# Kernel tuning notes

Measured on AMD Instinct MI355X. Metric: run time of the kernel, lower is better.

Reference implementation:

```python
import jax, jax.numpy as jnp
import numpy as np

VOCAB, IN, MEM, HID, CLS = 50000, 512, 512, 512, 5
N, K = 512, 4  # nodes per tree, max children (complete 4-ary tree)


def _build_children(n, k):
    # Complete k-ary heap, relabeled j = n-1-i so every child index < its parent
    # index (topological order for the scan). Pad missing children with n, which
    # indexes a permanent zero row in the state buffers (matches torch's zero
    # child_c/child_h for leaves: f*0 contributes nothing).
    ch = np.full((n, k), n, dtype=np.int32)
    for j in range(n):
        i = n - 1 - j
        for m in range(1, k + 1):
            c = k * i + m
            if c <= n - 1:
                ch[j, m - 1] = n - 1 - c
    return jnp.asarray(ch)


def setup_inputs() -> dict:
    key = jax.random.key(0)
    ks = jax.random.split(key, 16)
    s_in, s_mem, s_2m, s_h = IN ** -0.5, MEM ** -0.5, (2 * MEM) ** -0.5, HID ** -0.5
    emb = jax.random.normal(ks[0], (VOCAB, IN), jnp.float32)
    emb = emb.at[0].set(0.0)  # padding_idx=0
    inp = {
        "linputs": jax.random.randint(ks[1], (N,), 1, VOCAB, jnp.int32),
        "rinputs": jax.random.randint(ks[2], (N,), 1, VOCAB, jnp.int32),
        "lchildren": _build_children(N, K),
        "rchildren": _build_children(N, K),
        "emb": emb,
        "W_ioux": jax.random.normal(ks[3], (IN, 3 * MEM), jnp.float32) * s_in,
        "b_ioux": jnp.zeros((3 * MEM,), jnp.float32),
        "W_iouh": jax.random.normal(ks[4], (MEM, 3 * MEM), jnp.float32) * s_mem,
        "b_iouh": jnp.zeros((3 * MEM,), jnp.float32),
        "W_fx": jax.random.normal(ks[5], (IN, MEM), jnp.float32) * s_in,
        "b_fx": jnp.zeros((MEM,), jnp.float32),
        "W_fh": jax.random.normal(ks[6], (MEM, MEM), jnp.float32) * s_mem,
        "b_fh": jnp.zeros((MEM,), jnp.float32),
        "Wh": jax.random.normal(ks[7], (2 * MEM, HID), jnp.float32) * s_2m,
        "bh": jnp.zeros((HID,), jnp.float32),
        "Wp": jax.random.normal(ks[8], (HID, CLS), jnp.float32) * s_h,
        "bp": jnp.zeros((CLS,), jnp.float32),
    }
    return inp


def _childsum_encode(tokens, children, emb, W_ioux, b_ioux, W_iouh, b_iouh,
                     W_fx, b_fx, W_fh, b_fh):
    n, mem = tokens.shape[0], W_fh.shape[0]
    x = emb[tokens]                       # [N, IN]
    xiou = x @ W_ioux + b_ioux            # [N, 3M]  (input part, hoisted)
    xf = x @ W_fx + b_fx                  # [N, M]
    c0 = jnp.zeros((n + 1, mem), x.dtype)  # row n = permanent zero state
    h0 = jnp.zeros((n + 1, mem), x.dtype)

    def step(carry, inp):
        c_all, h_all = carry
        i, xiou_i, xf_i, ch = inp
        cc = c_all[ch]                    # [K, M]
        hh = h_all[ch]                    # [K, M]
        iou = xiou_i + hh.sum(0) @ W_iouh + b_iouh
        ig, og, ug = jnp.split(iou, 3)
        ig, og, ug = jax.nn.sigmoid(ig), jax.nn.sigmoid(og), jnp.tanh(ug)
        f = jax.nn.sigmoid(hh @ W_fh + b_fh + xf_i)   # [K, M]
        c = ig * ug + (f * cc).sum(0)
        h = og * jnp.tanh(c)
        return (c_all.at[i].set(c), h_all.at[i].set(h)), None

    idx = jnp.arange(n)
    (c_all, h_all), _ = jax.lax.scan(step, (c0, h0), (idx, xiou, xf, children))
    return c_all[n - 1][None, :], h_all[n - 1][None, :]  # root (c, h)


def reference(linputs, rinputs, lchildren, rchildren, emb,
              W_ioux, b_ioux, W_iouh, b_iouh, W_fx, b_fx, W_fh, b_fh,
              Wh, bh, Wp, bp):
    lc, _ = _childsum_encode(linputs, lchildren, emb, W_ioux, b_ioux,
                             W_iouh, b_iouh, W_fx, b_fx, W_fh, b_fh)
    rc, _ = _childsum_encode(rinputs, rchildren, emb, W_ioux, b_ioux,
                             W_iouh, b_iouh, W_fx, b_fx, W_fh, b_fh)
    # Similarity head (note: the torch model feeds CELL states lstate/rstate)
    vec = jnp.concatenate([lc * rc, jnp.abs(lc - rc)], axis=1)  # [1, 2M]
    hid = jax.nn.sigmoid(vec @ Wh + bh)
    return jax.nn.log_softmax(hid @ Wp + bp, axis=1)            # [1, CLS]
```

## Files before the change

### kernel.cpp

```cpp
#include <hip/hip_runtime.h>
#include <hip/hip_bf16.h>
#include <math.h>


typedef __attribute__((ext_vector_type(8))) __bf16 bf16x8;
typedef __attribute__((ext_vector_type(4))) float f32x4;

__device__ __forceinline__ float sigm(float x) { return 1.0f / (1.0f + __expf(-x)); }

__device__ __forceinline__ unsigned short f2bf(float f) {
    union { float f; unsigned int u; } v; v.f = f;
    unsigned int r = v.u + 0x7FFF + ((v.u >> 16) & 1);
    return (unsigned short)(r >> 16);
}
__device__ __forceinline__ float bf2f(unsigned short b) {
    union { unsigned int u; float f; } v; v.u = ((unsigned int)b) << 16;
    return v.f;
}
__device__ __forceinline__ f32x4 mfma16(bf16x8 a, bf16x8 b, f32x4 c) {
    return __builtin_amdgcn_mfma_f32_16x16x32_bf16(a, b, c, 0, 0, 0);
}
__device__ __forceinline__ bf16x8 load_f32_as_bf8(const float* p) {
    float4 x = *(const float4*)p;
    float4 y = *(const float4*)(p + 4);
    bf16x8 r;
    r[0] = (__bf16)x.x; r[1] = (__bf16)x.y; r[2] = (__bf16)x.z; r[3] = (__bf16)x.w;
    r[4] = (__bf16)y.x; r[5] = (__bf16)y.y; r[6] = (__bf16)y.z; r[7] = (__bf16)y.w;
    return r;
}

__device__ __forceinline__
void ttile(const float* __restrict__ src, int lds_, unsigned short* __restrict__ dst,
           int ldd, int k0, int n0, float (*ts)[33], int tid)
{
    const int tx = tid & 31, ty = tid >> 5;
#pragma unroll
    for (int i = 0; i < 4; ++i)
        ts[ty + 8 * i][tx] = src[(size_t)(k0 + ty + 8 * i) * lds_ + n0 + tx];
    __syncthreads();
#pragma unroll
    for (int i = 0; i < 4; ++i)
        dst[(size_t)(n0 + ty + 8 * i) * ldd + k0 + tx] = f2bf(ts[tx][ty + 8 * i]);
}

__global__ __launch_bounds__(256)
void prep(const float* __restrict__ W_iouh, const float* __restrict__ W_fh,
          const float* __restrict__ W_ioux, const float* __restrict__ W_fx,
          const float* __restrict__ Wh,
          unsigned short* __restrict__ WiouhT, unsigned short* __restrict__ WfhT,
          unsigned short* __restrict__ WxT, unsigned short* __restrict__ Whb,
          unsigned short* __restrict__ hbf, float* __restrict__ cbuf,
          float* __restrict__ hid_raw)
{
    __shared__ float ts[32][33];
    const int t = blockIdx.x, tid = threadIdx.x;
    if (t < 768) {
        ttile(W_iouh, 1536, WiouhT, 512, (t & 15) * 32, (t >> 4) * 32, ts, tid);
    } else if (t < 1024) {
        const int tt = t - 768;
        ttile(W_fh, 512, WfhT, 512, (tt & 15) * 32, (tt >> 4) * 32, ts, tid);
    } else if (t < 1792) {
        const int tt = t - 1024;
        ttile(W_ioux, 1536, WxT, 512, (tt & 15) * 32, (tt >> 4) * 32, ts, tid);
    } else if (t < 2048) {
        const int tt = t - 1792;
        ttile(W_fx, 512, WxT + (size_t)1536 * 512, 512, (tt & 15) * 32, (tt >> 4) * 32, ts, tid);
    } else if (t < 2304) {
        size_t base = (size_t)(t - 2048) * 2048 + tid;
#pragma unroll
        for (int i = 0; i < 8; ++i) Whb[base + 256 * i] = f2bf(Wh[base + 256 * i]);
    } else {
        for (int i = tid; i < 512; i += 256) {
            hbf[(size_t)512 * 512 + i] = 0;
            hbf[(size_t)1025 * 512 + i] = 0;
            cbuf[(size_t)512 * 512 + i] = 0.f;
            cbuf[(size_t)1025 * 512 + i] = 0.f;
            hid_raw[i] = 0.f;
        }
    }
}

__global__ __launch_bounds__(256)
void prege(const float* __restrict__ emb, const int* __restrict__ lin,
           const int* __restrict__ rin, const unsigned short* __restrict__ WxT,
           const float* __restrict__ b_ioux, const float* __restrict__ b_fx,
           unsigned short* __restrict__ xcat)
{
    const int mt = blockIdx.x & 31, nb = blockIdx.x >> 5;
    const int tid = threadIdx.x, w = tid >> 6, lane = tid & 63;
    const int m = lane & 15, q = lane >> 4;
    const int colbase = nb * 256 + w * 64;
    const int r0 = mt * 32 + m, r1 = r0 + 16;
    const int tok0 = (r0 < 512) ? lin[r0] : rin[r0 - 512];
    const int tok1 = (r1 < 512) ? lin[r1] : rin[r1 - 512];
    const float* A0 = emb + (size_t)tok0 * 512;
    const float* A1 = emb + (size_t)tok1 * 512;

    f32x4 acc[2][4];
#pragma unroll
    for (int i = 0; i < 2; ++i)
#pragma unroll
        for (int j = 0; j < 4; ++j) acc[i][j] = (f32x4){0.f, 0.f, 0.f, 0.f};

    for (int k0 = 0; k0 < 512; k0 += 32) {
        const int koff = k0 + q * 8;
        bf16x8 a0 = load_f32_as_bf8(A0 + koff);
        bf16x8 a1 = load_f32_as_bf8(A1 + koff);
#pragma unroll
        for (int jj = 0; jj < 4; ++jj) {
            bf16x8 b = *(const bf16x8*)(WxT + (size_t)(colbase + jj * 16 + m) * 512 + koff);
            acc[0][jj] = mfma16(a0, b, acc[0][jj]);
            acc[1][jj] = mfma16(a1, b, acc[1][jj]);
        }
    }
#pragma unroll
    for (int i = 0; i < 2; ++i)
#pragma unroll
        for (int jj = 0; jj < 4; ++jj)
#pragma unroll
            for (int rr = 0; rr < 4; ++rr) {
                const int R = mt * 32 + i * 16 + q * 4 + rr;
                const int col = colbase + jj * 16 + m;
                const float bias = (col < 1536) ? b_ioux[col] : b_fx[col - 1536];
                xcat[(size_t)R * 2048 + col] = f2bf(acc[i][jj][rr] + bias);
            }
}

__global__ __launch_bounds__(256)
void phase_gemm(const unsigned short* __restrict__ hbf,
                const int* __restrict__ lch, const int* __restrict__ rch,
                const unsigned short* __restrict__ WiouhT,
                const unsigned short* __restrict__ WfhT,
                const float* __restrict__ b_iouh, const float* __restrict__ b_fh,
                const unsigned short* __restrict__ xcat,
                float* __restrict__ ioub, float* __restrict__ fpre,
                int lo, int B, int nti1, int mti1, int mti2)
{
    const int B2 = 2 * B;
    const int tid = threadIdx.x, w = tid >> 6, lane = tid & 63;
    const int m = lane & 15, q = lane >> 4;
    int t = blockIdx.x;

    if (t < nti1) {
        const int mt = t % mti1, nb = t / mti1;
        const int colbase = nb * 256 + w * 64;
        const unsigned short* pA[2][4];
#pragma unroll
        for (int i = 0; i < 2; ++i) {
            const int r = mt * 32 + m + i * 16;
            int c[4] = {512, 512, 512, 512};
            int tree = 0;
            if (r < B2) {
                tree = (r >= B) ? 1 : 0;
                const int j = lo + r - tree * B;
                const int* ch = (tree ? rch : lch) + 4 * j;
                c[0] = ch[0]; c[1] = ch[1]; c[2] = ch[2]; c[3] = ch[3];
            }
            const unsigned short* hb = hbf + (size_t)tree * 513 * 512;
#pragma unroll
            for (int s = 0; s < 4; ++s) pA[i][s] = hb + (size_t)c[s] * 512;
        }
        f32x4 acc[2][4];
#pragma unroll
        for (int i = 0; i < 2; ++i)
#pragma unroll
            for (int j = 0; j < 4; ++j) acc[i][j] = (f32x4){0.f, 0.f, 0.f, 0.f};

        for (int k0 = 0; k0 < 512; k0 += 32) {
            const int koff = k0 + q * 8;
            bf16x8 af[2];
#pragma unroll
            for (int i = 0; i < 2; ++i) {
                float s[8] = {0.f, 0.f, 0.f, 0.f, 0.f, 0.f, 0.f, 0.f};
#pragma unroll
                for (int cc = 0; cc < 4; ++cc) {
                    bf16x8 v = *(const bf16x8*)(pA[i][cc] + koff);
#pragma unroll
                    for (int j = 0; j < 8; ++j) s[j] += (float)v[j];
                }
                bf16x8 a;
#pragma unroll
                for (int j = 0; j < 8; ++j) a[j] = (__bf16)s[j];
                af[i] = a;
            }
#pragma unroll
            for (int jj = 0; jj < 4; ++jj) {
                bf16x8 b = *(const bf16x8*)(WiouhT + (size_t)(colbase + jj * 16 + m) * 512 + koff);
                acc[0][jj] = mfma16(af[0], b, acc[0][jj]);
                acc[1][jj] = mfma16(af[1], b, acc[1][jj]);
            }
        }
#pragma unroll
        for (int i = 0; i < 2; ++i)
#pragma unroll
            for (int jj = 0; jj < 4; ++jj)
#pragma unroll
                for (int rr = 0; rr < 4; ++rr) {
                    const int R = mt * 32 + i * 16 + q * 4 + rr;
                    if (R < B2) {
                        const int tr = (R >= B) ? 1 : 0;
                        const int jR = lo + R - tr * B;
                        const int col = colbase + jj * 16 + m;
                        ioub[(size_t)R * 1536 + col] = acc[i][jj][rr] + b_iouh[col]
                            + bf2f(xcat[(size_t)(tr * 512 + jR) * 2048 + col]);
                    }
                }
    } else {
        t -= nti1;
        const int mt = t % mti2, nb = t / mti2;
        const int colbase = nb * 256 + w * 64;
        const unsigned short* pA[2];
#pragma unroll
        for (int i = 0; i < 2; ++i) {
            const int rf = mt * 32 + m + i * 16;
            int tree = 0, c = 512;
            if (rf < 4 * B2) {
                const int r = rf >> 2, s = rf & 3;
                tree = (r >= B) ? 1 : 0;
                const int j = lo + r - tree * B;
                c = ((tree ? rch : lch) + 4 * j)[s];
            }
            pA[i] = hbf + ((size_t)tree * 513 + c) * 512;
        }
        f32x4 acc[2][4];
#pragma unroll
        for (int i = 0; i < 2; ++i)
#pragma unroll
            for (int j = 0; j < 4; ++j) acc[i][j] = (f32x4){0.f, 0.f, 0.f, 0.f};

        for (int k0 = 0; k0 < 512; k0 += 32) {
            const int koff = k0 + q * 8;
            bf16x8 a0 = *(const bf16x8*)(pA[0] + koff);
            bf16x8 a1 = *(const bf16x8*)(pA[1] + koff);
#pragma unroll
            for (int jj = 0; jj < 4; ++jj) {
                bf16x8 b = *(const bf16x8*)(WfhT + (size_t)(colbase + jj * 16 + m) * 512 + koff);
                acc[0][jj] = mfma16(a0, b, acc[0][jj]);
                acc[1][jj] = mfma16(a1, b, acc[1][jj]);
            }
        }
#pragma unroll
        for (int i = 0; i < 2; ++i)
#pragma unroll
            for (int jj = 0; jj < 4; ++jj)
#pragma unroll
                for (int rr = 0; rr < 4; ++rr) {
                    const int R = mt * 32 + i * 16 + q * 4 + rr;
                    if (R < 4 * B2) {
                        const int rR = R >> 2;
                        const int tr = (rR >= B) ? 1 : 0;
                        const int jR = lo + rR - tr * B;
                        const int col = colbase + jj * 16 + m;
                        fpre[(size_t)R * 512 + col] = acc[i][jj][rr] + b_fh[col]
                            + bf2f(xcat[(size_t)(tr * 512 + jR) * 2048 + 1536 + col]);
                    }
                }
    }
}

__global__ __launch_bounds__(256)
void gating_k(const float* __restrict__ ioub, const float* __restrict__ fpre,
              const int* __restrict__ lch, const int* __restrict__ rch,
              float* __restrict__ cbuf, unsigned short* __restrict__ hbf,
              int lo, int B)
{
    const int r = blockIdx.x;
    const int tree = (r >= B) ? 1 : 0;
    const int j = lo + r - tree * B;
    const int* ch = (tree ? rch : lch) + 4 * j;
    const int c0 = ch[0], c1 = ch[1], c2 = ch[2], c3 = ch[3];
    float* cb = cbuf + (size_t)tree * 513 * 512;
    unsigned short* hb = hbf + (size_t)tree * 513 * 512;
    const float* ir = ioub + (size_t)r * 1536;
    const float* fr = fpre + (size_t)r * 4 * 512;
#pragma unroll
    for (int u = 0; u < 2; ++u) {
        const int col = threadIdx.x + u * 256;
        const float ig = sigm(ir[col]);
        const float og = sigm(ir[512 + col]);
        const float ug = tanhf(ir[1024 + col]);
        float cv = ig * ug
            + sigm(fr[col])        * cb[(size_t)c0 * 512 + col]
            + sigm(fr[512 + col])  * cb[(size_t)c1 * 512 + col]
            + sigm(fr[1024 + col]) * cb[(size_t)c2 * 512 + col]
            + sigm(fr[1536 + col]) * cb[(size_t)c3 * 512 + col];
        cb[(size_t)j * 512 + col] = cv;
        hb[(size_t)j * 512 + col] = f2bf(og * tanhf(cv));
    }
}

__global__ __launch_bounds__(256)
void head1(const float* __restrict__ cbuf, const unsigned short* __restrict__ Whb,
           float* __restrict__ hid_raw)
{
    __shared__ float red[4][64];
    const float* lc = cbuf + (size_t)511 * 512;
    const float* rc = cbuf + (size_t)(513 + 511) * 512;
    const int tid = threadIdx.x, w = tid >> 6, lane = tid & 63;
    const int cg = blockIdx.x & 7, kg = blockIdx.x >> 3;
    const int col = cg * 64 + lane;
    const int kbase = kg * 128 + w * 32;
    float acc = 0.f;
#pragma unroll 8
    for (int i = 0; i < 32; ++i) {
        const int k = kbase + i;
        float v;
        if (k < 512) v = lc[k] * rc[k];
        else { const int kk = k - 512; v = fabsf(lc[kk] - rc[kk]); }
        acc += v * bf2f(Whb[(size_t)k * 512 + col]);
    }
    red[w][lane] = acc;
    __syncthreads();
    if (w == 0)
        atomicAdd(&hid_raw[col], red[0][lane] + red[1][lane] + red[2][lane] + red[3][lane]);
}

__global__ __launch_bounds__(256)
void head2(const float* __restrict__ hid_raw, const float* __restrict__ bh,
           const float* __restrict__ Wp, const float* __restrict__ bp,
           float* __restrict__ out)
{
    __shared__ float red[4][5];
    const int tid = threadIdx.x, w = tid >> 6, lane = tid & 63;
    float a[5] = {0.f, 0.f, 0.f, 0.f, 0.f};
    for (int k = tid; k < 512; k += 256) {
        const float hv = sigm(hid_raw[k] + bh[k]);
#pragma unroll
        for (int cc = 0; cc < 5; ++cc) a[cc] += hv * Wp[(size_t)k * 5 + cc];
    }
#pragma unroll
    for (int cc = 0; cc < 5; ++cc)
        for (int off = 32; off; off >>= 1) a[cc] += __shfl_xor(a[cc], off, 64);
    if (lane == 0)
#pragma unroll
        for (int cc = 0; cc < 5; ++cc) red[w][cc] = a[cc];
    __syncthreads();
    if (tid == 0) {
        float lg[5], mx = -1e30f;
#pragma unroll
        for (int cc = 0; cc < 5; ++cc) {
            lg[cc] = red[0][cc] + red[1][cc] + red[2][cc] + red[3][cc] + bp[cc];
            mx = fmaxf(mx, lg[cc]);
        }
        float s = 0.f;
#pragma unroll
        for (int cc = 0; cc < 5; ++cc) s += __expf(lg[cc] - mx);
        const float lse = mx + __logf(s);
#pragma unroll
        for (int cc = 0; cc < 5; ++cc) out[cc] = lg[cc] - lse;
    }
}

extern "C" void kernel_launch(void* const* d_in, const int* in_sizes, int n_in,
                              void* d_out, int out_size, void* d_ws, size_t ws_size,
                              hipStream_t stream)
{
    const int*   lin     = (const int*)d_in[0];
    const int*   rin     = (const int*)d_in[1];
    const int*   lch     = (const int*)d_in[2];
    const int*   rch     = (const int*)d_in[3];
    const float* emb     = (const float*)d_in[4];
    const float* W_ioux  = (const float*)d_in[5];
    const float* b_ioux  = (const float*)d_in[6];
    const float* W_iouh  = (const float*)d_in[7];
    const float* b_iouh  = (const float*)d_in[8];
    const float* W_fx    = (const float*)d_in[9];
    const float* b_fx    = (const float*)d_in[10];
    const float* W_fh    = (const float*)d_in[11];
    const float* b_fh    = (const float*)d_in[12];
    const float* Wh      = (const float*)d_in[13];
    const float* bh      = (const float*)d_in[14];
    const float* Wp      = (const float*)d_in[15];
    const float* bp      = (const float*)d_in[16];
    float* out = (float*)d_out;
    (void)ws_size; (void)n_in; (void)in_sizes; (void)out_size;

    char* p = (char*)d_ws;
    unsigned short* WiouhT = (unsigned short*)p;            p += (size_t)1536 * 512 * 2;
    unsigned short* WfhT   = (unsigned short*)p;            p += (size_t)512 * 512 * 2;
    unsigned short* WxT    = (unsigned short*)p;            p += (size_t)2048 * 512 * 2;
    unsigned short* Whb    = (unsigned short*)p;            p += (size_t)1024 * 512 * 2;
    unsigned short* xcat   = (unsigned short*)p;            p += (size_t)1024 * 2048 * 2;
    unsigned short* hbf    = (unsigned short*)p;            p += (size_t)2 * 513 * 512 * 2;
    float*          cbuf   = (float*)p;                     p += (size_t)2 * 513 * 512 * 4;
    float*          ioub   = (float*)p;                     p += (size_t)512 * 1536 * 4;
    float*          fpre   = (float*)p;                     p += (size_t)2048 * 512 * 4;
    float*          hid_raw= (float*)p;                     p += (size_t)512 * 4;

    prep<<<2305, 256, 0, stream>>>(W_iouh, W_fh, W_ioux, W_fx, Wh,
                                   WiouhT, WfhT, WxT, Whb, hbf, cbuf, hid_raw);
    prege<<<256, 256, 0, stream>>>(emb, lin, rin, WxT, b_ioux, b_fx, xcat);

    static const int los[6] = {0, 171, 427, 491, 507, 511};
    static const int his[6] = {171, 427, 491, 507, 511, 512};
    for (int ph = 0; ph < 6; ++ph) {
        const int lo = los[ph], B = his[ph] - los[ph], B2 = 2 * B;
        const int mti1 = (B2 + 31) / 32;
        const int mti2 = (4 * B2 + 31) / 32;
        const int nti1 = mti1 * 6;
        const int nti2 = mti2 * 2;
        phase_gemm<<<nti1 + nti2, 256, 0, stream>>>(hbf, lch, rch, WiouhT, WfhT,
                                                    b_iouh, b_fh, xcat, ioub, fpre,
                                                    lo, B, nti1, mti1, mti2);
        gating_k<<<B2, 256, 0, stream>>>(ioub, fpre, lch, rch, cbuf, hbf, lo, B);
    }

    head1<<<64, 256, 0, stream>>>(cbuf, Whb, hid_raw);
    head2<<<1, 256, 0, stream>>>(hid_raw, bh, Wp, bp, out);
}
```

Measured before the change: 397.0 us.

## Fuse all phases into one cooperative persistent kernel with grid syncs

Replaces the sequence of about 16 kernel launches (prep, embedding GEMM, six phase GEMM/gating pairs, two head kernels) with a single cooperative kernel of 256 blocks that separates stages with grid.sync. It also special-cases the leaf phase, whose children are all zero, so it is computed directly from xcat without any GEMM. The final root gating and the classifier head run in one block. This removes launch gaps, but grid-wide barriers have their own cost, and the grid-strided loops can use the machine less fully than the old per-stage grid sizes did.

```diff
diff --git a/kernel.cpp b/kernel.cpp
--- a/kernel.cpp
+++ b/kernel.cpp
@@ -1,10 +1,14 @@
 #include <hip/hip_runtime.h>
-#include <hip/hip_bf16.h>
+#include <hip/hip_cooperative_groups.h>
 #include <math.h>
+
+namespace cg = cooperative_groups;
 
 
 typedef __attribute__((ext_vector_type(8))) __bf16 bf16x8;
 typedef __attribute__((ext_vector_type(4))) float f32x4;
+
+#define GRID 256
 
 __device__ __forceinline__ float sigm(float x) { return 1.0f / (1.0f + __expf(-x)); }
 
@@ -29,6 +33,16 @@
     return r;
 }
 
+struct Args {
+    const int   *lin, *rin, *lch, *rch;
+    const float *emb;
+    const float *W_ioux, *b_ioux, *W_iouh, *b_iouh;
+    const float *W_fx, *b_fx, *W_fh, *b_fh;
+    const float *Wh, *bh, *Wp, *bp;
+    unsigned short *WiouhT, *WfhT, *WxT, *Whb, *xcat, *hbf;
+    float *cbuf, *ioub, *fpre, *out;
+};
+
 __device__ __forceinline__
 void ttile(const float* __restrict__ src, int lds_, unsigned short* __restrict__ dst,
            int ldd, int k0, int n0, float (*ts)[33], int tid)
@@ -43,103 +57,12 @@
         dst[(size_t)(n0 + ty + 8 * i) * ldd + k0 + tx] = f2bf(ts[tx][ty + 8 * i]);
 }
 
-__global__ __launch_bounds__(256)
-void prep(const float* __restrict__ W_iouh, const float* __restrict__ W_fh,
-          const float* __restrict__ W_ioux, const float* __restrict__ W_fx,
-          const float* __restrict__ Wh,
-          unsigned short* __restrict__ WiouhT, unsigned short* __restrict__ WfhT,
-          unsigned short* __restrict__ WxT, unsigned short* __restrict__ Whb,
-          unsigned short* __restrict__ hbf, float* __restrict__ cbuf,
-          float* __restrict__ hid_raw)
-{
-    __shared__ float ts[32][33];
-    const int t = blockIdx.x, tid = threadIdx.x;
-    if (t < 768) {
-        ttile(W_iouh, 1536, WiouhT, 512, (t & 15) * 32, (t >> 4) * 32, ts, tid);
-    } else if (t < 1024) {
-        const int tt = t - 768;
-        ttile(W_fh, 512, WfhT, 512, (tt & 15) * 32, (tt >> 4) * 32, ts, tid);
-    } else if (t < 1792) {
-        const int tt = t - 1024;
-        ttile(W_ioux, 1536, WxT, 512, (tt & 15) * 32, (tt >> 4) * 32, ts, tid);
-    } else if (t < 2048) {
-        const int tt = t - 1792;
-        ttile(W_fx, 512, WxT + (size_t)1536 * 512, 512, (tt & 15) * 32, (tt >> 4) * 32, ts, tid);
-    } else if (t < 2304) {
-        size_t base = (size_t)(t - 2048) * 2048 + tid;
-#pragma unroll
-        for (int i = 0; i < 8; ++i) Whb[base + 256 * i] = f2bf(Wh[base + 256 * i]);
-    } else {
-        for (int i = tid; i < 512; i += 256) {
-            hbf[(size_t)512 * 512 + i] = 0;
-            hbf[(size_t)1025 * 512 + i] = 0;
-            cbuf[(size_t)512 * 512 + i] = 0.f;
-            cbuf[(size_t)1025 * 512 + i] = 0.f;
-            hid_raw[i] = 0.f;
-        }
-    }
-}
-
-__global__ __launch_bounds__(256)
-void prege(const float* __restrict__ emb, const int* __restrict__ lin,
-           const int* __restrict__ rin, const unsigned short* __restrict__ WxT,
-           const float* __restrict__ b_ioux, const float* __restrict__ b_fx,
-           unsigned short* __restrict__ xcat)
-{
-    const int mt = blockIdx.x & 31, nb = blockIdx.x >> 5;
-    const int tid = threadIdx.x, w = tid >> 6, lane = tid & 63;
-    const int m = lane & 15, q = lane >> 4;
-    const int colbase = nb * 256 + w * 64;
-    const int r0 = mt * 32 + m, r1 = r0 + 16;
-    const int tok0 = (r0 < 512) ? lin[r0] : rin[r0 - 512];
-    const int tok1 = (r1 < 512) ? lin[r1] : rin[r1 - 512];
-    const float* A0 = emb + (size_t)tok0 * 512;
-    const float* A1 = emb + (size_t)tok1 * 512;
-
-    f32x4 acc[2][4];
-#pragma unroll
-    for (int i = 0; i < 2; ++i)
-#pragma unroll
-        for (int j = 0; j < 4; ++j) acc[i][j] = (f32x4){0.f, 0.f, 0.f, 0.f};
-
-    for (int k0 = 0; k0 < 512; k0 += 32) {
-        const int koff = k0 + q * 8;
-        bf16x8 a0 = load_f32_as_bf8(A0 + koff);
-        bf16x8 a1 = load_f32_as_bf8(A1 + koff);
-#pragma unroll
-        for (int jj = 0; jj < 4; ++jj) {
-            bf16x8 b = *(const bf16x8*)(WxT + (size_t)(colbase + jj * 16 + m) * 512 + koff);
-            acc[0][jj] = mfma16(a0, b, acc[0][jj]);
-            acc[1][jj] = mfma16(a1, b, acc[1][jj]);
-        }
-    }
-#pragma unroll
-    for (int i = 0; i < 2; ++i)
-#pragma unroll
-        for (int jj = 0; jj < 4; ++jj)
-#pragma unroll
-            for (int rr = 0; rr < 4; ++rr) {
-                const int R = mt * 32 + i * 16 + q * 4 + rr;
-                const int col = colbase + jj * 16 + m;
-                const float bias = (col < 1536) ? b_ioux[col] : b_fx[col - 1536];
-                xcat[(size_t)R * 2048 + col] = f2bf(acc[i][jj][rr] + bias);
-            }
-}
-
-__global__ __launch_bounds__(256)
-void phase_gemm(const unsigned short* __restrict__ hbf,
-                const int* __restrict__ lch, const int* __restrict__ rch,
-                const unsigned short* __restrict__ WiouhT,
-                const unsigned short* __restrict__ WfhT,
-                const float* __restrict__ b_iouh, const float* __restrict__ b_fh,
-                const unsigned short* __restrict__ xcat,
-                float* __restrict__ ioub, float* __restrict__ fpre,
-                int lo, int B, int nti1, int mti1, int mti2)
+__device__ __forceinline__
+void gemm_task(int t, int lo, int B, int mti1, int nti1, int mti2, const Args& a)
 {
     const int B2 = 2 * B;
     const int tid = threadIdx.x, w = tid >> 6, lane = tid & 63;
     const int m = lane & 15, q = lane >> 4;
-    int t = blockIdx.x;
 
     if (t < nti1) {
         const int mt = t % mti1, nb = t / mti1;
@@ -153,10 +76,10 @@
             if (r < B2) {
                 tree = (r >= B) ? 1 : 0;
                 const int j = lo + r - tree * B;
-                const int* ch = (tree ? rch : lch) + 4 * j;
+                const int* ch = (tree ? a.rch : a.lch) + 4 * j;
                 c[0] = ch[0]; c[1] = ch[1]; c[2] = ch[2]; c[3] = ch[3];
             }
-            const unsigned short* hb = hbf + (size_t)tree * 513 * 512;
+            const unsigned short* hb = a.hbf + (size_t)tree * 513 * 512;
 #pragma unroll
             for (int s = 0; s < 4; ++s) pA[i][s] = hb + (size_t)c[s] * 512;
         }
@@ -178,14 +101,14 @@
 #pragma unroll
                     for (int j = 0; j < 8; ++j) s[j] += (float)v[j];
                 }
-                bf16x8 a;
-#pragma unroll
-                for (int j = 0; j < 8; ++j) a[j] = (__bf16)s[j];
-                af[i] = a;
+                bf16x8 av;
+#pragma unroll
+                for (int j = 0; j < 8; ++j) av[j] = (__bf16)s[j];
+                af[i] = av;
             }
 #pragma unroll
             for (int jj = 0; jj < 4; ++jj) {
-                bf16x8 b = *(const bf16x8*)(WiouhT + (size_t)(colbase + jj * 16 + m) * 512 + koff);
+                bf16x8 b = *(const bf16x8*)(a.WiouhT + (size_t)(colbase + jj * 16 + m) * 512 + koff);
                 acc[0][jj] = mfma16(af[0], b, acc[0][jj]);
                 acc[1][jj] = mfma16(af[1], b, acc[1][jj]);
             }
@@ -201,8 +124,8 @@
                         const int tr = (R >= B) ? 1 : 0;
                         const int jR = lo + R - tr * B;
                         const int col = colbase + jj * 16 + m;
-                        ioub[(size_t)R * 1536 + col] = acc[i][jj][rr] + b_iouh[col]
-                            + bf2f(xcat[(size_t)(tr * 512 + jR) * 2048 + col]);
+                        a.ioub[(size_t)R * 1536 + col] = acc[i][jj][rr] + a.b_iouh[col]
+                            + bf2f(a.xcat[(size_t)(tr * 512 + jR) * 2048 + col]);
                     }
                 }
     } else {
@@ -218,9 +141,9 @@
                 const int r = rf >> 2, s = rf & 3;
                 tree = (r >= B) ? 1 : 0;
                 const int j = lo + r - tree * B;
-                c = ((tree ? rch : lch) + 4 * j)[s];
-            }
-            pA[i] = hbf + ((size_t)tree * 513 + c) * 512;
+                c = ((tree ? a.rch : a.lch) + 4 * j)[s];
+            }
+            pA[i] = a.hbf + ((size_t)tree * 513 + c) * 512;
         }
         f32x4 acc[2][4];
 #pragma unroll
@@ -234,7 +157,7 @@
             bf16x8 a1 = *(const bf16x8*)(pA[1] + koff);
 #pragma unroll
             for (int jj = 0; jj < 4; ++jj) {
-                bf16x8 b = *(const bf16x8*)(WfhT + (size_t)(colbase + jj * 16 + m) * 512 + koff);
+                bf16x8 b = *(const bf16x8*)(a.WfhT + (size_t)(colbase + jj * 16 + m) * 512 + koff);
                 acc[0][jj] = mfma16(a0, b, acc[0][jj]);
                 acc[1][jj] = mfma16(a1, b, acc[1][jj]);
             }
@@ -251,31 +174,28 @@
                         const int tr = (rR >= B) ? 1 : 0;
                         const int jR = lo + rR - tr * B;
                         const int col = colbase + jj * 16 + m;
-                        fpre[(size_t)R * 512 + col] = acc[i][jj][rr] + b_fh[col]
-                            + bf2f(xcat[(size_t)(tr * 512 + jR) * 2048 + 1536 + col]);
+                        a.fpre[(size_t)R * 512 + col] = acc[i][jj][rr] + a.b_fh[col]
+                            + bf2f(a.xcat[(size_t)(tr * 512 + jR) * 2048 + 1536 + col]);
                     }
                 }
     }
 }
 
-__global__ __launch_bounds__(256)
-void gating_k(const float* __restrict__ ioub, const float* __restrict__ fpre,
-              const int* __restrict__ lch, const int* __restrict__ rch,
-              float* __restrict__ cbuf, unsigned short* __restrict__ hbf,
-              int lo, int B)
+__device__ __forceinline__
+void gate_row(int r, int lo, int B, const Args& a)
 {
-    const int r = blockIdx.x;
+    const int tid = threadIdx.x;
     const int tree = (r >= B) ? 1 : 0;
     const int j = lo + r - tree * B;
-    const int* ch = (tree ? rch : lch) + 4 * j;
+    const int* ch = (tree ? a.rch : a.lch) + 4 * j;
     const int c0 = ch[0], c1 = ch[1], c2 = ch[2], c3 = ch[3];
-    float* cb = cbuf + (size_t)tree * 513 * 512;
-    unsigned short* hb = hbf + (size_t)tree * 513 * 512;
-    const float* ir = ioub + (size_t)r * 1536;
-    const float* fr = fpre + (size_t)r * 4 * 512;
+    float* cb = a.cbuf + (size_t)tree * 513 * 512;
+    unsigned short* hb = a.hbf + (size_t)tree * 513 * 512;
+    const float* ir = a.ioub + (size_t)r * 1536;
+    const float* fr = a.fpre + (size_t)r * 4 * 512;
 #pragma unroll
     for (int u = 0; u < 2; ++u) {
-        const int col = threadIdx.x + u * 256;
+        const int col = tid + u * 256;
         const float ig = sigm(ir[col]);
         const float og = sigm(ir[512 + col]);
         const float ug = tanhf(ir[1024 + col]);
@@ -289,65 +209,192 @@
     }
 }
 
-__global__ __launch_bounds__(256)
-void head1(const float* __restrict__ cbuf, const unsigned short* __restrict__ Whb,
-           float* __restrict__ hid_raw)
+__global__ __launch_bounds__(256, 1)
+void mega(Args a)
 {
-    __shared__ float red[4][64];
-    const float* lc = cbuf + (size_t)511 * 512;
-    const float* rc = cbuf + (size_t)(513 + 511) * 512;
-    const int tid = threadIdx.x, w = tid >> 6, lane = tid & 63;
-    const int cg = blockIdx.x & 7, kg = blockIdx.x >> 3;
-    const int col = cg * 64 + lane;
-    const int kbase = kg * 128 + w * 32;
-    float acc = 0.f;
-#pragma unroll 8
-    for (int i = 0; i < 32; ++i) {
-        const int k = kbase + i;
-        float v;
-        if (k < 512) v = lc[k] * rc[k];
-        else { const int kk = k - 512; v = fabsf(lc[kk] - rc[kk]); }
-        acc += v * bf2f(Whb[(size_t)k * 512 + col]);
-    }
-    red[w][lane] = acc;
-    __syncthreads();
-    if (w == 0)
-        atomicAdd(&hid_raw[col], red[0][lane] + red[1][lane] + red[2][lane] + red[3][lane]);
-}
-
-__global__ __launch_bounds__(256)
-void head2(const float* __restrict__ hid_raw, const float* __restrict__ bh,
-           const float* __restrict__ Wp, const float* __restrict__ bp,
-           float* __restrict__ out)
-{
-    __shared__ float red[4][5];
-    const int tid = threadIdx.x, w = tid >> 6, lane = tid & 63;
-    float a[5] = {0.f, 0.f, 0.f, 0.f, 0.f};
-    for (int k = tid; k < 512; k += 256) {
-        const float hv = sigm(hid_raw[k] + bh[k]);
-#pragma unroll
-        for (int cc = 0; cc < 5; ++cc) a[cc] += hv * Wp[(size_t)k * 5 + cc];
-    }
-#pragma unroll
-    for (int cc = 0; cc < 5; ++cc)
-        for (int off = 32; off; off >>= 1) a[cc] += __shfl_xor(a[cc], off, 64);
-    if (lane == 0)
-#pragma unroll
-        for (int cc = 0; cc < 5; ++cc) red[w][cc] = a[cc];
-    __syncthreads();
-    if (tid == 0) {
-        float lg[5], mx = -1e30f;
-#pragma unroll
-        for (int cc = 0; cc < 5; ++cc) {
-            lg[cc] = red[0][cc] + red[1][cc] + red[2][cc] + red[3][cc] + bp[cc];
-            mx = fmaxf(mx, lg[cc]);
-        }
-        float s = 0.f;
-#pragma unroll
-        for (int cc = 0; cc < 5; ++cc) s += __expf(lg[cc] - mx);
-        const float lse = mx + __logf(s);
-#pragma unroll
-        for (int cc = 0; cc < 5; ++cc) out[cc] = lg[cc] - lse;
+    cg::grid_group grid = cg::this_grid();
+    const int tid = threadIdx.x, bid = blockIdx.x;
+    const int G = gridDim.x;
+    __shared__ float ts[32][33];
+
+    for (int t = bid; t < 2305; t += G) {
+        if (t < 768) {
+            ttile(a.W_iouh, 1536, a.WiouhT, 512, (t & 15) * 32, (t >> 4) * 32, ts, tid);
+        } else if (t < 1024) {
+            const int tt = t - 768;
+            ttile(a.W_fh, 512, a.WfhT, 512, (tt & 15) * 32, (tt >> 4) * 32, ts, tid);
+        } else if (t < 1792) {
+            const int tt = t - 1024;
+            ttile(a.W_ioux, 1536, a.WxT, 512, (tt & 15) * 32, (tt >> 4) * 32, ts, tid);
+        } else if (t < 2048) {
+            const int tt = t - 1792;
+            ttile(a.W_fx, 512, a.WxT + (size_t)1536 * 512, 512, (tt & 15) * 32, (tt >> 4) * 32, ts, tid);
+        } else if (t < 2304) {
+            size_t base = (size_t)(t - 2048) * 2048 + tid;
+#pragma unroll
+            for (int i = 0; i < 8; ++i) a.Whb[base + 256 * i] = f2bf(a.Wh[base + 256 * i]);
+        } else {
+            for (int i = tid; i < 512; i += 256) {
+                a.hbf[(size_t)512 * 512 + i] = 0;
+                a.hbf[(size_t)1025 * 512 + i] = 0;
+                a.cbuf[(size_t)512 * 512 + i] = 0.f;
+                a.cbuf[(size_t)1025 * 512 + i] = 0.f;
+            }
+        }
+        __syncthreads();
+    }
+    grid.sync();
+
+    for (int t = bid; t < 256; t += G) {
+        const int mt = t & 31, nb = t >> 5;
+        const int w = tid >> 6, lane = tid & 63;
+        const int m = lane & 15, q = lane >> 4;
+        const int colbase = nb * 256 + w * 64;
+        const int r0 = mt * 32 + m, r1 = r0 + 16;
+        const int tok0 = (r0 < 512) ? a.lin[r0] : a.rin[r0 - 512];
+        const int tok1 = (r1 < 512) ? a.lin[r1] : a.rin[r1 - 512];
+        const float* A0 = a.emb + (size_t)tok0 * 512;
+        const float* A1 = a.emb + (size_t)tok1 * 512;
+
+        f32x4 acc[2][4];
+#pragma unroll
+        for (int i = 0; i < 2; ++i)
+#pragma unroll
+            for (int j = 0; j < 4; ++j) acc[i][j] = (f32x4){0.f, 0.f, 0.f, 0.f};
+
+        for (int k0 = 0; k0 < 512; k0 += 32) {
+            const int koff = k0 + q * 8;
+            bf16x8 a0 = load_f32_as_bf8(A0 + koff);
+            bf16x8 a1 = load_f32_as_bf8(A1 + koff);
+#pragma unroll
+            for (int jj = 0; jj < 4; ++jj) {
+                bf16x8 b = *(const bf16x8*)(a.WxT + (size_t)(colbase + jj * 16 + m) * 512 + koff);
+                acc[0][jj] = mfma16(a0, b, acc[0][jj]);
+                acc[1][jj] = mfma16(a1, b, acc[1][jj]);
+            }
+        }
+#pragma unroll
+        for (int i = 0; i < 2; ++i)
+#pragma unroll
+            for (int jj = 0; jj < 4; ++jj)
+#pragma unroll
+                for (int rr = 0; rr < 4; ++rr) {
+                    const int R = mt * 32 + i * 16 + q * 4 + rr;
+                    const int col = colbase + jj * 16 + m;
+                    const float bias = (col < 1536) ? a.b_ioux[col] : a.b_fx[col - 1536];
+                    a.xcat[(size_t)R * 2048 + col] = f2bf(acc[i][jj][rr] + bias);
+                }
+    }
+    grid.sync();
+
+    for (int r = bid; r < 342; r += G) {
+        const int tree = (r >= 171) ? 1 : 0;
+        const int j = r - tree * 171;
+        const unsigned short* xr = a.xcat + (size_t)(tree * 512 + j) * 2048;
+        float* cb = a.cbuf + (size_t)tree * 513 * 512;
+        unsigned short* hb = a.hbf + (size_t)tree * 513 * 512;
+#pragma unroll
+        for (int u = 0; u < 2; ++u) {
+            const int col = tid + u * 256;
+            const float ig = sigm(bf2f(xr[col]) + a.b_iouh[col]);
+            const float og = sigm(bf2f(xr[512 + col]) + a.b_iouh[512 + col]);
+            const float ug = tanhf(bf2f(xr[1024 + col]) + a.b_iouh[1024 + col]);
+            const float cv = ig * ug;
+            cb[(size_t)j * 512 + col] = cv;
+            hb[(size_t)j * 512 + col] = f2bf(og * tanhf(cv));
+        }
+    }
+    grid.sync();
+
+    static const int los[5] = {171, 427, 491, 507, 511};
+    static const int Bs[5]  = {256, 64, 16, 4, 1};
+    for (int ph = 0; ph < 5; ++ph) {
+        const int lo = los[ph], B = Bs[ph], B2 = 2 * B;
+        const int mti1 = (B2 + 31) >> 5, mti2 = (4 * B2 + 31) >> 5;
+        const int nti1 = mti1 * 6;
+        const int ntot = nti1 + mti2 * 2;
+        for (int t = bid; t < ntot; t += G)
+            gemm_task(t, lo, B, mti1, nti1, mti2, a);
+        grid.sync();
+        if (ph < 4) {
+            for (int r = bid; r < B2; r += G)
+                gate_row(r, lo, B, a);
+            grid.sync();
+        }
+    }
+
+    if (bid == 0) {
+        __shared__ float sv[1024];
+#pragma unroll
+        for (int tree = 0; tree < 2; ++tree) {
+            const int* ch = (tree ? a.rch : a.lch) + 4 * 511;
+            const float* cb = a.cbuf + (size_t)tree * 513 * 512;
+            const float* ir = a.ioub + (size_t)tree * 1536;
+            const float* fr = a.fpre + (size_t)tree * 4 * 512;
+            const int c0 = ch[0], c1 = ch[1], c2 = ch[2], c3 = ch[3];
+#pragma unroll
+            for (int u = 0; u < 2; ++u) {
+                const int col = tid + u * 256;
+                const float ig = sigm(ir[col]);
+                const float ug = tanhf(ir[1024 + col]);
+                const float cv = ig * ug
+                    + sigm(fr[col])        * cb[(size_t)c0 * 512 + col]
+                    + sigm(fr[512 + col])  * cb[(size_t)c1 * 512 + col]
+                    + sigm(fr[1024 + col]) * cb[(size_t)c2 * 512 + col]
+                    + sigm(fr[1536 + col]) * cb[(size_t)c3 * 512 + col];
+                sv[tree * 512 + col] = cv;
+            }
+        }
+        __syncthreads();
+#pragma unroll
+        for (int u = 0; u < 2; ++u) {
+            const int k = tid + u * 256;
+            if (k < 512) {
+                const float lcv = sv[k], rcv = sv[512 + k];
+                sv[k] = lcv * rcv;
+                sv[512 + k] = fabsf(lcv - rcv);
+            }
+        }
+        __syncthreads();
+        float a0 = 0.f, a1 = 0.f;
+        for (int k = 0; k < 1024; ++k) {
+            const unsigned int wv = *(const unsigned int*)(a.Whb + (size_t)k * 512 + 2 * tid);
+            const float s = sv[k];
+            a0 += s * bf2f((unsigned short)(wv & 0xffffu));
+            a1 += s * bf2f((unsigned short)(wv >> 16));
+        }
+        const float h0 = sigm(a0 + a.bh[2 * tid]);
+        const float h1 = sigm(a1 + a.bh[2 * tid + 1]);
+        float lp[5];
+#pragma unroll
+        for (int cc = 0; cc < 5; ++cc)
+            lp[cc] = h0 * a.Wp[(size_t)(2 * tid) * 5 + cc]
+                   + h1 * a.Wp[(size_t)(2 * tid + 1) * 5 + cc];
+#pragma unroll
+        for (int cc = 0; cc < 5; ++cc)
+#pragma unroll
+            for (int off = 32; off; off >>= 1)
+                lp[cc] += __shfl_xor(lp[cc], off, 64);
+        __shared__ float red[4][5];
+        const int w = tid >> 6, lane = tid & 63;
+        if (lane == 0)
+#pragma unroll
+            for (int cc = 0; cc < 5; ++cc) red[w][cc] = lp[cc];
+        __syncthreads();
+        if (tid == 0) {
+            float lg[5], mx = -1e30f;
+#pragma unroll
+            for (int cc = 0; cc < 5; ++cc) {
+                lg[cc] = red[0][cc] + red[1][cc] + red[2][cc] + red[3][cc] + a.bp[cc];
+                mx = fmaxf(mx, lg[cc]);
+            }
+            float s = 0.f;
+#pragma unroll
+            for (int cc = 0; cc < 5; ++cc) s += __expf(lg[cc] - mx);
+            const float lse = mx + __logf(s);
+#pragma unroll
+            for (int cc = 0; cc < 5; ++cc) a.out[cc] = lg[cc] - lse;
+        }
     }
 }
 
@@ -355,56 +402,40 @@
                               void* d_out, int out_size, void* d_ws, size_t ws_size,
                               hipStream_t stream)
 {
-    const int*   lin     = (const int*)d_in[0];
-    const int*   rin     = (const int*)d_in[1];
-    const int*   lch     = (const int*)d_in[2];
-    const int*   rch     = (const int*)d_in[3];
-    const float* emb     = (const float*)d_in[4];
-    const float* W_ioux  = (const float*)d_in[5];
-    const float* b_ioux  = (const float*)d_in[6];
-    const float* W_iouh  = (const float*)d_in[7];
-    const float* b_iouh  = (const float*)d_in[8];
-    const float* W_fx    = (const float*)d_in[9];
-    const float* b_fx    = (const float*)d_in[10];
-    const float* W_fh    = (const float*)d_in[11];
-    const float* b_fh    = (const float*)d_in[12];
-    const float* Wh      = (const float*)d_in[13];
-    const float* bh      = (const float*)d_in[14];
-    const float* Wp      = (const float*)d_in[15];
-    const float* bp      = (const float*)d_in[16];
-    float* out = (float*)d_out;
     (void)ws_size; (void)n_in; (void)in_sizes; (void)out_size;
 
+    Args ha;
+    ha.lin     = (const int*)d_in[0];
+    ha.rin     = (const int*)d_in[1];
+    ha.lch     = (const int*)d_in[2];
+    ha.rch     = (const int*)d_in[3];
+    ha.emb     = (const float*)d_in[4];
+    ha.W_ioux  = (const float*)d_in[5];
+    ha.b_ioux  = (const float*)d_in[6];
+    ha.W_iouh  = (const float*)d_in[7];
+    ha.b_iouh  = (const float*)d_in[8];
+    ha.W_fx    = (const float*)d_in[9];
+    ha.b_fx    = (const float*)d_in[10];
+    ha.W_fh    = (const float*)d_in[11];
+    ha.b_fh    = (const float*)d_in[12];
+    ha.Wh      = (const float*)d_in[13];
+    ha.bh      = (const float*)d_in[14];
+    ha.Wp      = (const float*)d_in[15];
+    ha.bp      = (const float*)d_in[16];
+    ha.out     = (float*)d_out;
+
     char* p = (char*)d_ws;
-    unsigned short* WiouhT = (unsigned short*)p;            p += (size_t)1536 * 512 * 2;
-    unsigned short* WfhT   = (unsigned short*)p;            p += (size_t)512 * 512 * 2;
-    unsigned short* WxT    = (unsigned short*)p;            p += (size_t)2048 * 512 * 2;
-    unsigned short* Whb    = (unsigned short*)p;            p += (size_t)1024 * 512 * 2;
-    unsigned short* xcat   = (unsigned short*)p;            p += (size_t)1024 * 2048 * 2;
-    unsigned short* hbf    = (unsigned short*)p;            p += (size_t)2 * 513 * 512 * 2;
-    float*          cbuf   = (float*)p;                     p += (size_t)2 * 513 * 512 * 4;
-    float*          ioub   = (float*)p;                     p += (size_t)512 * 1536 * 4;
-    float*          fpre   = (float*)p;                     p += (size_t)2048 * 512 * 4;
-    float*          hid_raw= (float*)p;                     p += (size_t)512 * 4;
-
-    prep<<<2305, 256, 0, stream>>>(W_iouh, W_fh, W_ioux, W_fx, Wh,
-                                   WiouhT, WfhT, WxT, Whb, hbf, cbuf, hid_raw);
-    prege<<<256, 256, 0, stream>>>(emb, lin, rin, WxT, b_ioux, b_fx, xcat);
-
-    static const int los[6] = {0, 171, 427, 491, 507, 511};
-    static const int his[6] = {171, 427, 491, 507, 511, 512};
-    for (int ph = 0; ph < 6; ++ph) {
-        const int lo = los[ph], B = his[ph] - los[ph], B2 = 2 * B;
-        const int mti1 = (B2 + 31) / 32;
-        const int mti2 = (4 * B2 + 31) / 32;
-        const int nti1 = mti1 * 6;
-        const int nti2 = mti2 * 2;
-        phase_gemm<<<nti1 + nti2, 256, 0, stream>>>(hbf, lch, rch, WiouhT, WfhT,
-                                                    b_iouh, b_fh, xcat, ioub, fpre,
-                                                    lo, B, nti1, mti1, mti2);
-        gating_k<<<B2, 256, 0, stream>>>(ioub, fpre, lch, rch, cbuf, hbf, lo, B);
-    }
-
-    head1<<<64, 256, 0, stream>>>(cbuf, Whb, hid_raw);
-    head2<<<1, 256, 0, stream>>>(hid_raw, bh, Wp, bp, out);
-}
+    ha.WiouhT = (unsigned short*)p;  p += (size_t)1536 * 512 * 2;
+    ha.WfhT   = (unsigned short*)p;  p += (size_t)512 * 512 * 2;
+    ha.WxT    = (unsigned short*)p;  p += (size_t)2048 * 512 * 2;
+    ha.Whb    = (unsigned short*)p;  p += (size_t)1024 * 512 * 2;
+    ha.xcat   = (unsigned short*)p;  p += (size_t)1024 * 2048 * 2;
+    ha.hbf    = (unsigned short*)p;  p += (size_t)2 * 513 * 512 * 2;
+    ha.cbuf   = (float*)p;           p += (size_t)2 * 513 * 512 * 4;
+    ha.ioub   = (float*)p;           p += (size_t)512 * 1536 * 4;
+    ha.fpre   = (float*)p;           p += (size_t)2048 * 512 * 4;
+
+    void* kargs[] = { &ha };
+    hipLaunchCooperativeKernel((const void*)mega, dim3(GRID), dim3(256),
+                               kargs, 0, stream);
+}
```

New measurement: 735.4 us. 85.2% more time.
